# Kernel tuning notes

Hardware: AMD Instinct MI355X
Metric: run time of the kernel (lower is better)

The kernel has to match this reference:

```python
import jax, jax.numpy as jnp
import numpy as np

N_HEAD = 16
N_EMBD = 1024

def setup_inputs() -> dict:
    key = jax.random.key(0)
    ks = jax.random.split(key, 5)
    C = N_EMBD
    x = jax.random.normal(ks[0], (4, 2048, C), dtype=jnp.float32)
    s = 1.0 / np.sqrt(C)
    W_attn = jax.random.normal(ks[1], (C, 3 * C), dtype=jnp.float32) * s
    b_attn = jax.random.normal(ks[2], (3 * C,), dtype=jnp.float32) * 0.02
    W_proj = jax.random.normal(ks[3], (C, C), dtype=jnp.float32) * s
    b_proj = jax.random.normal(ks[4], (C,), dtype=jnp.float32) * 0.02
    return {"x": x, "W_attn": W_attn, "b_attn": b_attn, "W_proj": W_proj, "b_proj": b_proj}

def reference(x, W_attn, b_attn, W_proj, b_proj):
    B, T, C = x.shape
    H = C // N_HEAD
    qkv = x @ W_attn + b_attn  # [B,T,3C]
    q, k, v = jnp.split(qkv, 3, axis=2)
    # [B,T,C] -> [B,nh,T,H]
    q = q.reshape(B, T, N_HEAD, H).transpose(0, 2, 1, 3)
    k = k.reshape(B, T, N_HEAD, H).transpose(0, 2, 1, 3)
    v = v.reshape(B, T, N_HEAD, H).transpose(0, 2, 1, 3)
    att = jnp.einsum('bhqd,bhkd->bhqk', q, k) * (1.0 / np.sqrt(H).astype(np.float32))
    causal = jnp.tril(jnp.ones((T, T), dtype=bool))  # [T,T]
    att = jnp.where(causal, att, -jnp.inf)
    att = jax.nn.softmax(att, axis=-1)
    y = jnp.einsum('bhqk,bhkd->bhqd', att, v)
    y = y.transpose(0, 2, 1, 3).reshape(B, T, C)
    return y @ W_proj + b_proj
```

## Files before the change

### kernel.cpp

```cpp
#include <hip/hip_runtime.h>
#include <math.h>

#define T_LEN 2048
#define C_DIM 1024
#define C3    3072
#define NHEAD 16
#define HDIM  64

typedef __attribute__((ext_vector_type(8))) __bf16 bf16x8;
typedef __attribute__((ext_vector_type(8))) unsigned short u16x8;
typedef __attribute__((ext_vector_type(4))) float f32x4;
typedef __attribute__((ext_vector_type(2))) unsigned int u32x2;
typedef unsigned short ushort_t;

#define QK_SCALE 0.180336878f

#if defined(__has_builtin)
#if __has_builtin(__builtin_amdgcn_exp2f)
#define FAST_EXP2(x) __builtin_amdgcn_exp2f(x)
#endif
#if __has_builtin(__builtin_amdgcn_permlane32_swap) && __has_builtin(__builtin_amdgcn_permlane16_swap)
#define HAVE_PERMLANE_SWAP 1
#endif
#endif
#ifndef FAST_EXP2
#define FAST_EXP2(x) exp2f(x)
#endif

__device__ __forceinline__ ushort_t f2bf(float f) {
    unsigned int u = __float_as_uint(f);
    unsigned int r = (u + 0x7FFFu + ((u >> 16) & 1u)) >> 16;
    return (ushort_t)r;
}

#define GLL16(g, l) __builtin_amdgcn_global_load_lds( \
    (const __attribute__((address_space(1))) void*)(g), \
    (__attribute__((address_space(3))) void*)(l), 16, 0, 0)

__global__ __launch_bounds__(256) void prep_inputs(
    const float* __restrict__ x, ushort_t* __restrict__ xb,
    const float* __restrict__ W1, ushort_t* __restrict__ Wt1,
    const float* __restrict__ W2, ushort_t* __restrict__ Wt2)
{
    __shared__ float t[64][65];
    const int bx = blockIdx.x;
    if (bx < 8192) {
        const int i = bx * 256 + threadIdx.x;
        const float4 v = ((const float4*)x)[i];
        ushort4 o;
        o.x = f2bf(v.x); o.y = f2bf(v.y); o.z = f2bf(v.z); o.w = f2bf(v.w);
        ((ushort4*)xb)[i] = o;
        return;
    }
    const float* W; ushort_t* Wt; int N, n0, k0;
    if (bx < 8960) {
        const int tt = bx - 8192;
        W = W1; Wt = Wt1; N = C3;
        n0 = (tt % 48) * 64; k0 = (tt / 48) * 64;
    } else {
        const int tt = bx - 8960;
        W = W2; Wt = Wt2; N = C_DIM;
        n0 = (tt % 16) * 64; k0 = (tt / 16) * 64;
    }
    const int K = C_DIM;
    const int c = threadIdx.x & 63, r4 = threadIdx.x >> 6;
#pragma unroll
    for (int i = 0; i < 16; i++) {
        int r = i * 4 + r4;
        t[r][c] = W[(size_t)(k0 + r) * N + n0 + c];
    }
    __syncthreads();
#pragma unroll
    for (int i = 0; i < 16; i++) {
        int r = i * 4 + r4;
        Wt[(size_t)(n0 + r) * K + k0 + c] = f2bf(t[c][r]);
    }
}

template <bool OUT_BF16, bool QSCALE>
__global__ __launch_bounds__(256, 3) void gemm_bt_mfma(
    const ushort_t* __restrict__ A, const ushort_t* __restrict__ Bt,
    const float* __restrict__ bias, void* __restrict__ Cv,
    int M, int N, int K)
{
    __shared__ ushort_t Alds[128 * 64];
    __shared__ ushort_t Blds[128 * 64];

    const int tid = threadIdx.x;
    const int bid = blockIdx.x;
    const int jj = bid >> 3;
    const int m0 = (((bid & 7) << 3) | (jj & 7)) * 128;
    const int n0 = (jj >> 3) * 128;
    const int w = tid >> 6;
    const int ln = tid & 63;
    const int quad = ln >> 4;
    const int r16 = ln & 15;
    const int wr0 = (w & 1) * 64;
    const int wc0 = (w >> 1) * 64;

    f32x4 acc[4][4] = {};

    const int srow = tid >> 3;
    const int csrc8 = ((tid & 7) ^ (srow & 7)) * 8;
    const int sw = r16 & 7;

    for (int k0 = 0; k0 < K; k0 += 64) {
#pragma unroll
        for (int rr = 0; rr < 4; rr++) {
            const ushort_t* ga = A + (size_t)(m0 + rr * 32 + srow) * K + k0 + csrc8;
            GLL16(ga, Alds + rr * 2048 + tid * 8);
            const ushort_t* gb = Bt + (size_t)(n0 + rr * 32 + srow) * K + k0 + csrc8;
            GLL16(gb, Blds + rr * 2048 + tid * 8);
        }
        __syncthreads();

#pragma unroll
        for (int s = 0; s < 2; s++) {
            const int cpos = ((4 * s + quad) ^ sw) * 8;
            bf16x8 af[4], bfr[4];
#pragma unroll
            for (int i = 0; i < 4; i++)
                af[i] = *(const bf16x8*)(Alds + (wr0 + i * 16 + r16) * 64 + cpos);
#pragma unroll
            for (int j = 0; j < 4; j++)
                bfr[j] = *(const bf16x8*)(Blds + (wc0 + j * 16 + r16) * 64 + cpos);
#pragma unroll
            for (int i = 0; i < 4; i++)
#pragma unroll
                for (int j = 0; j < 4; j++)
                    acc[i][j] = __builtin_amdgcn_mfma_f32_16x16x32_bf16(
                        af[i], bfr[j], acc[i][j], 0, 0, 0);
        }
        __syncthreads();
    }

    const float scl = (QSCALE && n0 < C_DIM) ? QK_SCALE : 1.0f;

#pragma unroll
    for (int j = 0; j < 4; j++) {
        const int col = n0 + wc0 + j * 16 + r16;
        const float bv = bias[col];
#pragma unroll
        for (int i = 0; i < 4; i++) {
            const int rowb = m0 + wr0 + i * 16 + quad * 4;
#pragma unroll
            for (int r = 0; r < 4; r++) {
                const float v = (acc[i][j][r] + bv) * scl;
                if (OUT_BF16)
                    ((ushort_t*)Cv)[(size_t)(rowb + r) * N + col] = f2bf(v);
                else
                    ((float*)Cv)[(size_t)(rowb + r) * N + col] = v;
            }
        }
    }
}

__global__ __launch_bounds__(256) void transpose_v(
    const ushort_t* __restrict__ qkv, ushort_t* __restrict__ vtg)
{
    __shared__ ushort_t Ts[64][72];
    const int t0 = blockIdx.x * 64;
    const int bh = blockIdx.y;
    const int b = bh >> 4, h = bh & 15;
    const ushort_t* src = qkv + (size_t)b * T_LEN * C3 + 2 * C_DIM + h * HDIM;
    const int tid = threadIdx.x;
    {
        const int r = tid >> 2, cs = (tid & 3) * 16;
        *(u16x8*)(&Ts[r][cs])     = *(const u16x8*)(src + (size_t)(t0 + r) * C3 + cs);
        *(u16x8*)(&Ts[r][cs + 8]) = *(const u16x8*)(src + (size_t)(t0 + r) * C3 + cs + 8);
    }
    __syncthreads();
    {
        const int d = tid >> 2, ts0 = (tid & 3) * 16;
        ushort_t* dst = vtg + ((size_t)bh * HDIM + d) * T_LEN + t0 + ts0;
        u16x8 o0, o1;
#pragma unroll
        for (int j = 0; j < 8; j++) o0[j] = Ts[ts0 + j][d];
#pragma unroll
        for (int j = 0; j < 8; j++) o1[j] = Ts[ts0 + 8 + j][d];
        *(u16x8*)dst = o0;
        *(u16x8*)(dst + 8) = o1;
    }
}


__device__ __forceinline__ void mask_diag(f32x4 (&s)[4], int qloc, int quad)
{
#pragma unroll
    for (int mb = 0; mb < 4; mb++)
#pragma unroll
        for (int r = 0; r < 4; r++)
            if (mb * 16 + quad * 4 + r > qloc) s[mb][r] = -1e30f;
}

__device__ __forceinline__ void softmax_exchange(
    f32x4 (&s)[4], float& lacc, bf16x8 (&bp)[2])
{
    unsigned int pk[4][2];
#pragma unroll
    for (int mb = 0; mb < 4; mb++) {
        const float p0 = FAST_EXP2(s[mb][0]);
        const float p1 = FAST_EXP2(s[mb][1]);
        const float p2 = FAST_EXP2(s[mb][2]);
        const float p3 = FAST_EXP2(s[mb][3]);
        lacc += (p0 + p1) + (p2 + p3);
        pk[mb][0] = __builtin_amdgcn_perm(__float_as_uint(p1), __float_as_uint(p0), 0x07060302u);
        pk[mb][1] = __builtin_amdgcn_perm(__float_as_uint(p3), __float_as_uint(p2), 0x07060302u);
    }
#pragma unroll
    for (int s2 = 0; s2 < 2; s2++) {
        uint4 t;
#pragma unroll
        for (int u = 0; u < 2; u++) {
            unsigned int A = pk[2 * s2][u], B = pk[2 * s2 + 1][u];
            unsigned int out1, out2;
#ifdef HAVE_PERMLANE_SWAP
            u32x2 r1 = __builtin_amdgcn_permlane32_swap(A, B, false, false);
            u32x2 r2 = __builtin_amdgcn_permlane16_swap(r1.x, r1.y, false, false);
            out1 = r2.x; out2 = r2.y;
#else
            asm volatile("s_nop 1\n\t"
                         "v_permlane32_swap_b32 %0, %1\n\t"
                         "s_nop 1\n\t"
                         "v_permlane16_swap_b32 %0, %1"
                         : "+v"(A), "+v"(B));
            out1 = A; out2 = B;
#endif
            if (u == 0) { t.x = out1; t.z = out2; }
            else        { t.y = out1; t.w = out2; }
        }
        bp[s2] = *(bf16x8*)&t;
    }
}

#define STAGE_K(kt_, buf_) do {                                               \
    const int _k0 = (kt_) * 64;                                               \
    const int _bo = (buf_) * 4096;                                            \
    _Pragma("unroll")                                                         \
    for (int rr = 0; rr < 2; rr++) {                                          \
        const ushort_t* gk = basek + (size_t)(_k0 + rr * 32 + srow) * C3 + csrc8; \
        GLL16(gk, Ks + _bo + rr * 2048 + tid * 8);                            \
    }                                                                         \
} while (0)

#define STAGE_V(kt_, buf_) do {                                               \
    const int _k0 = (kt_) * 64;                                               \
    const int _bo = (buf_) * 4096;                                            \
    _Pragma("unroll")                                                         \
    for (int rr = 0; rr < 2; rr++) {                                          \
        const ushort_t* gv = vrow + (size_t)(rr * 32 + srow) * T_LEN + _k0 + csrc8; \
        GLL16(gv, Vs + _bo + rr * 2048 + tid * 8);                            \
    }                                                                         \
} while (0)

__global__ __launch_bounds__(256, 4) void attn_flash_mfma5(
    const ushort_t* __restrict__ qkv, const ushort_t* __restrict__ vtg,
    ushort_t* __restrict__ y)
{
    __shared__ ushort_t Ks[2 * 64 * 64];
    __shared__ ushort_t Vs[2 * 64 * 64];

    const int bid = blockIdx.x;
    const int i = (bid >> 3) >> 3;
    const int bh = (bid & 7) * 8 + ((bid >> 3) & 7);
    const int b = bh >> 4, h = bh & 15;
    const int qA0 = i * 64;
    const int qB0 = (31 - i) * 64;
    const int lastkt = 31 - i;

    const int tid = threadIdx.x;
    const int w = tid >> 6;
    const int ln = tid & 63;
    const int quad = ln >> 4;
    const int r16 = ln & 15;
    const int qloc = w * 16 + r16;
    const int sw = r16 & 7;

    const int srow = tid >> 3;
    const int csrc8 = ((tid & 7) ^ (srow & 7)) * 8;
    const int cpos0 = (quad ^ sw) * 8;

    const ushort_t* baseq = qkv + (size_t)b * T_LEN * C3 + h * HDIM;
    const ushort_t* basek = baseq + C_DIM;
    const ushort_t* vrow = vtg + (size_t)bh * HDIM * T_LEN;

    STAGE_K(0, 0);
    STAGE_V(0, 0);

    bf16x8 aqA[2], aqB[2];
#pragma unroll
    for (int s = 0; s < 2; s++) {
        aqA[s] = *(const bf16x8*)(baseq + (size_t)(qA0 + qloc) * C3 + s * 32 + quad * 8);
        aqB[s] = *(const bf16x8*)(baseq + (size_t)(qB0 + qloc) * C3 + s * 32 + quad * 8);
    }

    f32x4 oA[4] = {}, oB[4] = {};
    float lA = 0.0f, lB = 0.0f;

    for (int kt = 0; kt <= lastkt; kt++) {
        __syncthreads();

        if (kt < lastkt) {
            STAGE_K(kt + 1, (kt + 1) & 1);
            STAGE_V(kt + 1, (kt + 1) & 1);
        }

        const int kb = (kt & 1) * 4096;

        if (kt <= i) {
            f32x4 sA[4] = {}, sB[4] = {};
#pragma unroll
            for (int s = 0; s < 2; s++)
#pragma unroll
                for (int mb = 0; mb < 4; mb++) {
                    const bf16x8 ak = *(const bf16x8*)(Ks + kb + (mb * 16 + r16) * 64 + (cpos0 ^ (s * 32)));
                    sA[mb] = __builtin_amdgcn_mfma_f32_16x16x32_bf16(ak, aqA[s], sA[mb], 0, 0, 0);
                    sB[mb] = __builtin_amdgcn_mfma_f32_16x16x32_bf16(ak, aqB[s], sB[mb], 0, 0, 0);
                }
            if (kt == i) mask_diag(sA, qloc, quad);
            bf16x8 bpA[2], bpB[2];
            softmax_exchange(sA, lA, bpA);
            softmax_exchange(sB, lB, bpB);
#pragma unroll
            for (int s = 0; s < 2; s++)
#pragma unroll
                for (int mb = 0; mb < 4; mb++) {
                    const bf16x8 av = *(const bf16x8*)(Vs + kb + (mb * 16 + r16) * 64 + (cpos0 ^ (s * 32)));
                    oA[mb] = __builtin_amdgcn_mfma_f32_16x16x32_bf16(av, bpA[s], oA[mb], 0, 0, 0);
                    oB[mb] = __builtin_amdgcn_mfma_f32_16x16x32_bf16(av, bpB[s], oB[mb], 0, 0, 0);
                }
        } else {
            f32x4 sB[4] = {};
#pragma unroll
            for (int s = 0; s < 2; s++)
#pragma unroll
                for (int mb = 0; mb < 4; mb++) {
                    const bf16x8 ak = *(const bf16x8*)(Ks + kb + (mb * 16 + r16) * 64 + (cpos0 ^ (s * 32)));
                    sB[mb] = __builtin_amdgcn_mfma_f32_16x16x32_bf16(ak, aqB[s], sB[mb], 0, 0, 0);
                }
            if (kt == lastkt) mask_diag(sB, qloc, quad);
            bf16x8 bpB[2];
            softmax_exchange(sB, lB, bpB);
#pragma unroll
            for (int s = 0; s < 2; s++)
#pragma unroll
                for (int mb = 0; mb < 4; mb++) {
                    const bf16x8 av = *(const bf16x8*)(Vs + kb + (mb * 16 + r16) * 64 + (cpos0 ^ (s * 32)));
                    oB[mb] = __builtin_amdgcn_mfma_f32_16x16x32_bf16(av, bpB[s], oB[mb], 0, 0, 0);
                }
        }
    }

    lA += __shfl_xor(lA, 16); lA += __shfl_xor(lA, 32);
    lB += __shfl_xor(lB, 16); lB += __shfl_xor(lB, 32);
    {
        const float invA = 1.0f / lA;
        ushort_t* yp = y + ((size_t)(b * T_LEN + qA0 + qloc)) * C_DIM + h * HDIM;
#pragma unroll
        for (int mb = 0; mb < 4; mb++) {
            ushort4 o;
            o.x = f2bf(oA[mb][0] * invA);
            o.y = f2bf(oA[mb][1] * invA);
            o.z = f2bf(oA[mb][2] * invA);
            o.w = f2bf(oA[mb][3] * invA);
            *(ushort4*)(yp + mb * 16 + quad * 4) = o;
        }
    }
    {
        const float invB = 1.0f / lB;
        ushort_t* yp = y + ((size_t)(b * T_LEN + qB0 + qloc)) * C_DIM + h * HDIM;
#pragma unroll
        for (int mb = 0; mb < 4; mb++) {
            ushort4 o;
            o.x = f2bf(oB[mb][0] * invB);
            o.y = f2bf(oB[mb][1] * invB);
            o.z = f2bf(oB[mb][2] * invB);
            o.w = f2bf(oB[mb][3] * invB);
            *(ushort4*)(yp + mb * 16 + quad * 4) = o;
        }
    }
}

extern "C" void kernel_launch(void* const* d_in, const int* in_sizes, int n_in,
                              void* d_out, int out_size, void* d_ws, size_t ws_size,
                              hipStream_t stream)
{
    const float* x      = (const float*)d_in[0];
    const float* W_attn = (const float*)d_in[1];
    const float* b_attn = (const float*)d_in[2];
    const float* W_proj = (const float*)d_in[3];
    const float* b_proj = (const float*)d_in[4];
    float* out = (float*)d_out;

    const int M = 4 * T_LEN;
    char* ws = (char*)d_ws;
    ushort_t* qkv = (ushort_t*)ws;
    ushort_t* xb  = (ushort_t*)(ws + 50331648);
    ushort_t* Wt1 = (ushort_t*)(ws + 67108864);
    ushort_t* yb  = (ushort_t*)(ws + 73400320);
    ushort_t* Wt2 = (ushort_t*)(ws + 90177536);
    ushort_t* vtg = (ushort_t*)(ws + 92274688);

    prep_inputs<<<9216, 256, 0, stream>>>(x, xb, W_attn, Wt1, W_proj, Wt2);

    gemm_bt_mfma<true, true><<<dim3((M / 128) * (C3 / 128)), 256, 0, stream>>>(
        xb, Wt1, b_attn, qkv, M, C3, C_DIM);

    transpose_v<<<dim3(T_LEN / 64, 4 * NHEAD), 256, 0, stream>>>(qkv, vtg);

    attn_flash_mfma5<<<dim3(1024), 256, 0, stream>>>(qkv, vtg, yb);

    gemm_bt_mfma<false, false><<<dim3((M / 128) * (C_DIM / 128)), 256, 0, stream>>>(
        yb, Wt2, b_proj, out, M, C_DIM, C_DIM);
}
```

Before: 254.0 us.

## Software-pipeline QK^T for the next tile behind PV with deeper prefetch

Restructures the flash-attention loop so the QK^T MFMAs for tile kt+1 are issued right after the PV MFMAs for tile kt. This lets matrix work overlap the softmax dependency chain. Prefetch distance grows to two tiles, so V gets a third LDS buffer and the single barrier moves to the end of each iteration. It costs extra LDS per block, which may reduce occupancy under the 4-blocks-per-CU launch bound, and keeping two sets of score registers live raises register pressure.

```diff
diff --git a/kernel.cpp b/kernel.cpp
--- a/kernel.cpp
+++ b/kernel.cpp
@@ -243,13 +243,12 @@
     }                                                                         \
 } while (0)
 
-#define STAGE_V(kt_, buf_) do {                                               \
+#define STAGE_V(kt_, vofs_) do {                                              \
     const int _k0 = (kt_) * 64;                                               \
-    const int _bo = (buf_) * 4096;                                            \
     _Pragma("unroll")                                                         \
     for (int rr = 0; rr < 2; rr++) {                                          \
         const ushort_t* gv = vrow + (size_t)(rr * 32 + srow) * T_LEN + _k0 + csrc8; \
-        GLL16(gv, Vs + _bo + rr * 2048 + tid * 8);                            \
+        GLL16(gv, Vs + (vofs_) + rr * 2048 + tid * 8);                        \
     }                                                                         \
 } while (0)
 
@@ -258,7 +257,7 @@
     ushort_t* __restrict__ y)
 {
     __shared__ ushort_t Ks[2 * 64 * 64];
-    __shared__ ushort_t Vs[2 * 64 * 64];
+    __shared__ ushort_t Vs[3 * 64 * 64];
 
     const int bid = blockIdx.x;
     const int i = (bid >> 3) >> 3;
@@ -286,6 +285,8 @@
 
     STAGE_K(0, 0);
     STAGE_V(0, 0);
+    STAGE_K(1, 1);
+    STAGE_V(1, 4096);
 
     bf16x8 aqA[2], aqB[2];
 #pragma unroll
@@ -297,26 +298,28 @@
     f32x4 oA[4] = {}, oB[4] = {};
     float lA = 0.0f, lB = 0.0f;
 
+    __syncthreads();
+
+    f32x4 sA[4] = {}, sB[4] = {};
+#pragma unroll
+    for (int s = 0; s < 2; s++)
+#pragma unroll
+        for (int mb = 0; mb < 4; mb++) {
+            const bf16x8 ak = *(const bf16x8*)(Ks + (mb * 16 + r16) * 64 + (cpos0 ^ (s * 32)));
+            sA[mb] = __builtin_amdgcn_mfma_f32_16x16x32_bf16(ak, aqA[s], sA[mb], 0, 0, 0);
+            sB[mb] = __builtin_amdgcn_mfma_f32_16x16x32_bf16(ak, aqB[s], sB[mb], 0, 0, 0);
+        }
+
+    int v0 = 0, v1 = 4096, v2 = 8192;
+
     for (int kt = 0; kt <= lastkt; kt++) {
-        __syncthreads();
-
-        if (kt < lastkt) {
-            STAGE_K(kt + 1, (kt + 1) & 1);
-            STAGE_V(kt + 1, (kt + 1) & 1);
-        }
-
-        const int kb = (kt & 1) * 4096;
+        if (kt + 2 <= lastkt) {
+            STAGE_K(kt + 2, kt & 1);
+            STAGE_V(kt + 2, v2);
+        }
+        const int kbn = ((kt + 1) & 1) * 4096;
 
         if (kt <= i) {
-            f32x4 sA[4] = {}, sB[4] = {};
-#pragma unroll
-            for (int s = 0; s < 2; s++)
-#pragma unroll
-                for (int mb = 0; mb < 4; mb++) {
-                    const bf16x8 ak = *(const bf16x8*)(Ks + kb + (mb * 16 + r16) * 64 + (cpos0 ^ (s * 32)));
-                    sA[mb] = __builtin_amdgcn_mfma_f32_16x16x32_bf16(ak, aqA[s], sA[mb], 0, 0, 0);
-                    sB[mb] = __builtin_amdgcn_mfma_f32_16x16x32_bf16(ak, aqB[s], sB[mb], 0, 0, 0);
-                }
             if (kt == i) mask_diag(sA, qloc, quad);
             bf16x8 bpA[2], bpB[2];
             softmax_exchange(sA, lA, bpA);
@@ -325,19 +328,25 @@
             for (int s = 0; s < 2; s++)
 #pragma unroll
                 for (int mb = 0; mb < 4; mb++) {
-                    const bf16x8 av = *(const bf16x8*)(Vs + kb + (mb * 16 + r16) * 64 + (cpos0 ^ (s * 32)));
+                    const bf16x8 av = *(const bf16x8*)(Vs + v0 + (mb * 16 + r16) * 64 + (cpos0 ^ (s * 32)));
                     oA[mb] = __builtin_amdgcn_mfma_f32_16x16x32_bf16(av, bpA[s], oA[mb], 0, 0, 0);
                     oB[mb] = __builtin_amdgcn_mfma_f32_16x16x32_bf16(av, bpB[s], oB[mb], 0, 0, 0);
                 }
+            if (kt < lastkt) {
+                const bool dualn = (kt + 1 <= i);
+#pragma unroll
+                for (int mb = 0; mb < 4; mb++) { sB[mb] = (f32x4){}; sA[mb] = (f32x4){}; }
+#pragma unroll
+                for (int s = 0; s < 2; s++)
+#pragma unroll
+                    for (int mb = 0; mb < 4; mb++) {
+                        const bf16x8 ak = *(const bf16x8*)(Ks + kbn + (mb * 16 + r16) * 64 + (cpos0 ^ (s * 32)));
+                        sB[mb] = __builtin_amdgcn_mfma_f32_16x16x32_bf16(ak, aqB[s], sB[mb], 0, 0, 0);
+                        if (dualn)
+                            sA[mb] = __builtin_amdgcn_mfma_f32_16x16x32_bf16(ak, aqA[s], sA[mb], 0, 0, 0);
+                    }
+            }
         } else {
-            f32x4 sB[4] = {};
-#pragma unroll
-            for (int s = 0; s < 2; s++)
-#pragma unroll
-                for (int mb = 0; mb < 4; mb++) {
-                    const bf16x8 ak = *(const bf16x8*)(Ks + kb + (mb * 16 + r16) * 64 + (cpos0 ^ (s * 32)));
-                    sB[mb] = __builtin_amdgcn_mfma_f32_16x16x32_bf16(ak, aqB[s], sB[mb], 0, 0, 0);
-                }
             if (kt == lastkt) mask_diag(sB, qloc, quad);
             bf16x8 bpB[2];
             softmax_exchange(sB, lB, bpB);
@@ -345,10 +354,25 @@
             for (int s = 0; s < 2; s++)
 #pragma unroll
                 for (int mb = 0; mb < 4; mb++) {
-                    const bf16x8 av = *(const bf16x8*)(Vs + kb + (mb * 16 + r16) * 64 + (cpos0 ^ (s * 32)));
+                    const bf16x8 av = *(const bf16x8*)(Vs + v0 + (mb * 16 + r16) * 64 + (cpos0 ^ (s * 32)));
                     oB[mb] = __builtin_amdgcn_mfma_f32_16x16x32_bf16(av, bpB[s], oB[mb], 0, 0, 0);
                 }
-        }
+            if (kt < lastkt) {
+#pragma unroll
+                for (int mb = 0; mb < 4; mb++) sB[mb] = (f32x4){};
+#pragma unroll
+                for (int s = 0; s < 2; s++)
+#pragma unroll
+                    for (int mb = 0; mb < 4; mb++) {
+                        const bf16x8 ak = *(const bf16x8*)(Ks + kbn + (mb * 16 + r16) * 64 + (cpos0 ^ (s * 32)));
+                        sB[mb] = __builtin_amdgcn_mfma_f32_16x16x32_bf16(ak, aqB[s], sB[mb], 0, 0, 0);
+                    }
+            }
+        }
+
+        const int vt = v0; v0 = v1; v1 = v2; v2 = vt;
+
+        __syncthreads();
     }
 
     lA += __shfl_xor(lA, 16); lA += __shfl_xor(lA, 32);
```

New measurement: 791.5 us. 212% more time.

## Replace paired causal q-tiles with one q-tile per block, longest first

Applied to the files above, without the earlier changes.

The attention kernel no longer pairs q-tile i with q-tile 31-i inside one block. Each block now handles a single 64-row q-tile, and blocks are ordered so the longest causal rows launch first, doubling the grid to 2048 blocks. The launch-bounds occupancy hint is also dropped. This cuts per-block register pressure and relies on longest-first scheduling for load balance, but each K/V tile is now loaded once per q-tile instead of shared between two, and there are more blocks.

```diff
diff --git a/kernel.cpp b/kernel.cpp
--- a/kernel.cpp
+++ b/kernel.cpp
@@ -253,7 +253,7 @@
     }                                                                         \
 } while (0)
 
-__global__ __launch_bounds__(256, 4) void attn_flash_mfma5(
+__global__ __launch_bounds__(256) void attn_flash_mfma5(
     const ushort_t* __restrict__ qkv, const ushort_t* __restrict__ vtg,
     ushort_t* __restrict__ y)
 {
@@ -261,12 +261,15 @@
     __shared__ ushort_t Vs[2 * 64 * 64];
 
     const int bid = blockIdx.x;
-    const int i = (bid >> 3) >> 3;
-    const int bh = (bid & 7) * 8 + ((bid >> 3) & 7);
+    const int xcd = bid & 7;
+    const int kk = bid >> 3;
+    const int head = kk & 7;
+    const int ii = kk >> 3;
+    const int i = 31 - ii;
+    const int bh = xcd * 8 + head;
     const int b = bh >> 4, h = bh & 15;
-    const int qA0 = i * 64;
-    const int qB0 = (31 - i) * 64;
-    const int lastkt = 31 - i;
+    const int q0 = i * 64;
+    const int lastkt = i;
 
     const int tid = threadIdx.x;
     const int w = tid >> 6;
@@ -287,15 +290,13 @@
     STAGE_K(0, 0);
     STAGE_V(0, 0);
 
-    bf16x8 aqA[2], aqB[2];
-#pragma unroll
-    for (int s = 0; s < 2; s++) {
-        aqA[s] = *(const bf16x8*)(baseq + (size_t)(qA0 + qloc) * C3 + s * 32 + quad * 8);
-        aqB[s] = *(const bf16x8*)(baseq + (size_t)(qB0 + qloc) * C3 + s * 32 + quad * 8);
-    }
-
-    f32x4 oA[4] = {}, oB[4] = {};
-    float lA = 0.0f, lB = 0.0f;
+    bf16x8 aq[2];
+#pragma unroll
+    for (int s = 0; s < 2; s++)
+        aq[s] = *(const bf16x8*)(baseq + (size_t)(q0 + qloc) * C3 + s * 32 + quad * 8);
+
+    f32x4 o[4] = {};
+    float l = 0.0f;
 
     for (int kt = 0; kt <= lastkt; kt++) {
         __syncthreads();
@@ -307,77 +308,37 @@
 
         const int kb = (kt & 1) * 4096;
 
-        if (kt <= i) {
-            f32x4 sA[4] = {}, sB[4] = {};
-#pragma unroll
-            for (int s = 0; s < 2; s++)
-#pragma unroll
-                for (int mb = 0; mb < 4; mb++) {
-                    const bf16x8 ak = *(const bf16x8*)(Ks + kb + (mb * 16 + r16) * 64 + (cpos0 ^ (s * 32)));
-                    sA[mb] = __builtin_amdgcn_mfma_f32_16x16x32_bf16(ak, aqA[s], sA[mb], 0, 0, 0);
-                    sB[mb] = __builtin_amdgcn_mfma_f32_16x16x32_bf16(ak, aqB[s], sB[mb], 0, 0, 0);
-                }
-            if (kt == i) mask_diag(sA, qloc, quad);
-            bf16x8 bpA[2], bpB[2];
-            softmax_exchange(sA, lA, bpA);
-            softmax_exchange(sB, lB, bpB);
-#pragma unroll
-            for (int s = 0; s < 2; s++)
-#pragma unroll
-                for (int mb = 0; mb < 4; mb++) {
-                    const bf16x8 av = *(const bf16x8*)(Vs + kb + (mb * 16 + r16) * 64 + (cpos0 ^ (s * 32)));
-                    oA[mb] = __builtin_amdgcn_mfma_f32_16x16x32_bf16(av, bpA[s], oA[mb], 0, 0, 0);
-                    oB[mb] = __builtin_amdgcn_mfma_f32_16x16x32_bf16(av, bpB[s], oB[mb], 0, 0, 0);
-                }
-        } else {
-            f32x4 sB[4] = {};
-#pragma unroll
-            for (int s = 0; s < 2; s++)
-#pragma unroll
-                for (int mb = 0; mb < 4; mb++) {
-                    const bf16x8 ak = *(const bf16x8*)(Ks + kb + (mb * 16 + r16) * 64 + (cpos0 ^ (s * 32)));
-                    sB[mb] = __builtin_amdgcn_mfma_f32_16x16x32_bf16(ak, aqB[s], sB[mb], 0, 0, 0);
-                }
-            if (kt == lastkt) mask_diag(sB, qloc, quad);
-            bf16x8 bpB[2];
-            softmax_exchange(sB, lB, bpB);
-#pragma unroll
-            for (int s = 0; s < 2; s++)
-#pragma unroll
-                for (int mb = 0; mb < 4; mb++) {
-                    const bf16x8 av = *(const bf16x8*)(Vs + kb + (mb * 16 + r16) * 64 + (cpos0 ^ (s * 32)));
-                    oB[mb] = __builtin_amdgcn_mfma_f32_16x16x32_bf16(av, bpB[s], oB[mb], 0, 0, 0);
-                }
-        }
-    }
-
-    lA += __shfl_xor(lA, 16); lA += __shfl_xor(lA, 32);
-    lB += __shfl_xor(lB, 16); lB += __shfl_xor(lB, 32);
-    {
-        const float invA = 1.0f / lA;
-        ushort_t* yp = y + ((size_t)(b * T_LEN + qA0 + qloc)) * C_DIM + h * HDIM;
-#pragma unroll
-        for (int mb = 0; mb < 4; mb++) {
-            ushort4 o;
-            o.x = f2bf(oA[mb][0] * invA);
-            o.y = f2bf(oA[mb][1] * invA);
-            o.z = f2bf(oA[mb][2] * invA);
-            o.w = f2bf(oA[mb][3] * invA);
-            *(ushort4*)(yp + mb * 16 + quad * 4) = o;
-        }
-    }
-    {
-        const float invB = 1.0f / lB;
-        ushort_t* yp = y + ((size_t)(b * T_LEN + qB0 + qloc)) * C_DIM + h * HDIM;
-#pragma unroll
-        for (int mb = 0; mb < 4; mb++) {
-            ushort4 o;
-            o.x = f2bf(oB[mb][0] * invB);
-            o.y = f2bf(oB[mb][1] * invB);
-            o.z = f2bf(oB[mb][2] * invB);
-            o.w = f2bf(oB[mb][3] * invB);
-            *(ushort4*)(yp + mb * 16 + quad * 4) = o;
-        }
+        f32x4 s4[4] = {};
+#pragma unroll
+        for (int s = 0; s < 2; s++)
+#pragma unroll
+            for (int mb = 0; mb < 4; mb++) {
+                const bf16x8 ak = *(const bf16x8*)(Ks + kb + (mb * 16 + r16) * 64 + (cpos0 ^ (s * 32)));
+                s4[mb] = __builtin_amdgcn_mfma_f32_16x16x32_bf16(ak, aq[s], s4[mb], 0, 0, 0);
+            }
+        if (kt == lastkt) mask_diag(s4, qloc, quad);
+        bf16x8 bp[2];
+        softmax_exchange(s4, l, bp);
+#pragma unroll
+        for (int s = 0; s < 2; s++)
+#pragma unroll
+            for (int mb = 0; mb < 4; mb++) {
+                const bf16x8 av = *(const bf16x8*)(Vs + kb + (mb * 16 + r16) * 64 + (cpos0 ^ (s * 32)));
+                o[mb] = __builtin_amdgcn_mfma_f32_16x16x32_bf16(av, bp[s], o[mb], 0, 0, 0);
+            }
+    }
+
+    l += __shfl_xor(l, 16); l += __shfl_xor(l, 32);
+    const float inv = 1.0f / l;
+    ushort_t* yp = y + ((size_t)(b * T_LEN + q0 + qloc)) * C_DIM + h * HDIM;
+#pragma unroll
+    for (int mb = 0; mb < 4; mb++) {
+        ushort4 ov;
+        ov.x = f2bf(o[mb][0] * inv);
+        ov.y = f2bf(o[mb][1] * inv);
+        ov.z = f2bf(o[mb][2] * inv);
+        ov.w = f2bf(o[mb][3] * inv);
+        *(ushort4*)(yp + mb * 16 + quad * 4) = ov;
     }
 }
 
@@ -408,7 +369,7 @@
 
     transpose_v<<<dim3(T_LEN / 64, 4 * NHEAD), 256, 0, stream>>>(qkv, vtg);
 
-    attn_flash_mfma5<<<dim3(1024), 256, 0, stream>>>(qkv, vtg, yb);
+    attn_flash_mfma5<<<dim3(2048), 256, 0, stream>>>(qkv, vtg, yb);
 
     gemm_bt_mfma<false, false><<<dim3((M / 128) * (C_DIM / 128)), 256, 0, stream>>>(
         yb, Wt2, b_proj, out, M, C_DIM, C_DIM);
```

Result: faster. 228.6 us (-10.0%).
